# Optimization experiments

Hardware: AMD Instinct MI355X
Metric: run time of the kernel (lower is better)

Reference implementation:

```python
import jax, jax.numpy as jnp
import numpy as np

N = 100_000      # nodes
E = 800_000      # edges
NF = 32          # node_feature_size
EF = 32          # edge_feature_size
L = 64           # layer_size
ENTRY = NF + EF          # 64, input width of node_mlp_1
SECOND = NF + L          # 96, input width of node_mlp_2
SLOPE = 0.1              # leakiness
EPS = 1e-5               # BatchNorm1d eps


def _bn(h, g, b):
    # BatchNorm1d in training mode: batch mean, biased variance
    m = h.mean(0)
    v = ((h - m) ** 2).mean(0)
    return (h - m) * jax.lax.rsqrt(v + EPS) * g + b


def _lrelu(h):
    return jnp.where(h > 0, h, SLOPE * h)


def setup_inputs() -> dict:
    key = jax.random.key(0)
    ks = jax.random.split(key, 16)

    def w(k, i, o):
        return (jax.random.normal(k, (i, o), jnp.float32) / np.float32(np.sqrt(i)))

    def bvec(k, o):
        return jax.random.normal(k, (o,), jnp.float32) * 0.01

    inp = {
        "x": jax.random.normal(ks[0], (N, NF), jnp.float32),
        "edge_index": jax.random.randint(ks[1], (2, E), 0, N),
        "edge_attr": jax.random.normal(ks[2], (E, EF), jnp.float32),
        "u": jax.random.normal(ks[3], (1, 4), jnp.float32),
        "batch": jnp.zeros((N,), jnp.int32),
        # node_mlp_1 params
        "m1_g1": jnp.ones((ENTRY,), jnp.float32), "m1_b1": jnp.zeros((ENTRY,), jnp.float32),
        "m1_w1": w(ks[4], ENTRY, L), "m1_c1": bvec(ks[5], L),
        "m1_g2": jnp.ones((L,), jnp.float32), "m1_b2": jnp.zeros((L,), jnp.float32),
        "m1_w2": w(ks[6], L, L), "m1_c2": bvec(ks[7], L),
        "m1_g3": jnp.ones((L,), jnp.float32), "m1_b3": jnp.zeros((L,), jnp.float32),
        "m1_w3": w(ks[8], L, L), "m1_c3": bvec(ks[9], L),
        # node_mlp_2 params
        "m2_g1": jnp.ones((SECOND,), jnp.float32), "m2_b1": jnp.zeros((SECOND,), jnp.float32),
        "m2_w1": w(ks[10], SECOND, SECOND), "m2_c1": bvec(ks[11], SECOND),
        "m2_g2": jnp.ones((SECOND,), jnp.float32), "m2_b2": jnp.zeros((SECOND,), jnp.float32),
        "m2_w2": w(ks[12], SECOND, SECOND), "m2_c2": bvec(ks[13], SECOND),
        "m2_g3": jnp.ones((SECOND,), jnp.float32), "m2_b3": jnp.zeros((SECOND,), jnp.float32),
        "m2_w3": w(ks[14], SECOND, NF), "m2_c3": bvec(ks[15], NF),
    }
    return inp


def reference(x, edge_index, edge_attr, u, batch,
              m1_g1, m1_b1, m1_w1, m1_c1,
              m1_g2, m1_b2, m1_w2, m1_c2,
              m1_g3, m1_b3, m1_w3, m1_c3,
              m2_g1, m2_b1, m2_w1, m2_c1,
              m2_g2, m2_b2, m2_w2, m2_c2,
              m2_g3, m2_b3, m2_w3, m2_c3):
    row, col = edge_index[0], edge_index[1]
    # gather source node features, concat with edge features  [E, ENTRY]
    h = jnp.concatenate([x[row], edge_attr], axis=1)
    # node_mlp_1: BN -> Linear -> LReLU -> BN -> Linear -> LReLU -> BN -> Linear
    h = _lrelu(_bn(h, m1_g1, m1_b1) @ m1_w1 + m1_c1)
    h = _lrelu(_bn(h, m1_g2, m1_b2) @ m1_w2 + m1_c2)
    h = _bn(h, m1_g3, m1_b3) @ m1_w3 + m1_c3
    # scatter-sum back to destination nodes  [N, L]
    agg = jax.ops.segment_sum(h, col, num_segments=x.shape[0])
    # node_mlp_2 on [x, agg]  [N, SECOND]
    h2 = jnp.concatenate([x, agg], axis=1)
    h2 = _lrelu(_bn(h2, m2_g1, m2_b1) @ m2_w1 + m2_c1)
    h2 = _lrelu(_bn(h2, m2_g2, m2_b2) @ m2_w2 + m2_c2)
    out = _bn(h2, m2_g3, m2_b3) @ m2_w3 + m2_c3  # [N, NF]
    return out
```

## Files before the change

### kernel.cpp

```cpp
#include <hip/hip_runtime.h>


typedef unsigned short u16;
typedef __bf16  bf16x8  __attribute__((ext_vector_type(8)));
typedef float   floatx4 __attribute__((ext_vector_type(4)));

#define NBIN 8

__device__ __forceinline__ float bf2f(u16 u) {
  union { float f; unsigned int i; } v; v.i = ((unsigned int)u) << 16; return v.f;
}
__device__ __forceinline__ u16 f2bf(float f) {
  union { float f; unsigned int i; } v; v.f = f;
  unsigned int x = v.i;
  return (u16)((x + 0x7fffu + ((x >> 16) & 1u)) >> 16);
}
__device__ __forceinline__ bf16x8 ldb8(const u16* p) {
  return *reinterpret_cast<const bf16x8*>(p);
}
__device__ __forceinline__ floatx4 mfma16(bf16x8 a, bf16x8 b, floatx4 c) {
  return __builtin_amdgcn_mfma_f32_16x16x32_bf16(a, b, c, 0, 0, 0);
}
__device__ __forceinline__ float loadf(const void* p, long idx, int mode) {
  return mode ? bf2f(((const u16*)p)[idx]) : ((const float*)p)[idx];
}
__device__ __forceinline__ bf16x8 load8(const void* p, long idx, int mode) {
  if (mode) return ldb8((const u16*)p + idx);
  const float* f = (const float*)p + idx;
  bf16x8 r;
#pragma unroll
  for (int j = 0; j < 8; j++) r[j] = (__bf16)f[j];
  return r;
}

__global__ void detect_kernel(const u16* __restrict__ x, int* __restrict__ modep) {
  __shared__ int cnt;
  if (threadIdx.x == 0) cnt = 0;
  __syncthreads();
  int weird = 0;
  for (int i = threadIdx.x; i < 1024; i += blockDim.x) {
    unsigned e = (x[i] >> 7) & 0xFFu;
    if (e == 0xFFu || e >= 0x90u || (e != 0u && e < 0x60u)) weird++;
  }
  atomicAdd(&cnt, weird);
  __syncthreads();
  if (threadIdx.x == 0) *modep = (cnt > 128) ? 0 : 1;
}
// ... 17 lines not shown
  __syncthreads();
  int src = 0;
  for (int off = 1; off < 1024; off <<= 1) {
    int t = tmp[src][tid];
    if (tid >= off) t += tmp[src][tid - off];
    tmp[1 - src][tid] = t;
    src = 1 - src;
    __syncthreads();
  }
  if (i < n) excl[i] = tmp[src][tid] - v;
  if (tid == 1023) bsum[blockIdx.x] = tmp[src][1023];
}

__global__ void scan2_kernel(int* __restrict__ bsum, int nb,
                             int* __restrict__ offsets, int N, int E) {
  if (threadIdx.x == 0) {
    int run = 0;
    for (int i = 0; i < nb; i++) { int v = bsum[i]; bsum[i] = run; run += v; }
    offsets[N] = E;
  }
}

__global__ void scan3_kernel(int* __restrict__ offsets, const int* __restrict__ bsum,
                             int n, int* __restrict__ cursor) {
  int i = blockIdx.x * 1024 + threadIdx.x;
  if (i < n) {
    int v = offsets[i] + bsum[blockIdx.x];
    offsets[i] = v;
    cursor[i] = v;
  }
}

__global__ void scatter_kernel(const int* __restrict__ col, int E,
                               int* __restrict__ cursor, int* __restrict__ ipos,
                               int* __restrict__ nodeof) {
  for (int e = blockIdx.x * blockDim.x + threadIdx.x; e < E;
       e += gridDim.x * blockDim.x) {
    int d = col[e];
    int pos = atomicAdd(&cursor[d], 1);
    ipos[e] = pos;
    nodeof[pos] = d;
  }
}

__global__ void statsXW_kernel(const void* __restrict__ x, const int* __restrict__ odeg,
                               int N, float* __restrict__ stats0,
                               float* __restrict__ statsB0,
                               const int* __restrict__ modep) {
  const int mode = *modep;
  const int c = threadIdx.x & 31, rs = threadIdx.x >> 5;
  float s = 0.f, q = 0.f, ws = 0.f, wq = 0.f;
  for (long r = (long)blockIdx.x * 8 + rs; r < N; r += (long)gridDim.x * 8) {
    float v = loadf(x, r * 32 + c, mode);
    float w = (float)odeg[r];
    s += v; q += v * v;
    ws += w * v; wq += w * v * v;
  }
  __shared__ float sm[4][256];
  sm[0][threadIdx.x] = s; sm[1][threadIdx.x] = q;
  sm[2][threadIdx.x] = ws; sm[3][threadIdx.x] = wq;
  __syncthreads();
  if (threadIdx.x < 32) {
    for (int i = 1; i < 8; i++) {
      s  += sm[0][i * 32 + c]; q  += sm[1][i * 32 + c];
      ws += sm[2][i * 32 + c]; wq += sm[3][i * 32 + c];
    }
    const int bin = blockIdx.x & (NBIN - 1);
    atomicAdd(statsB0 + bin * 192 + c, s);
    atomicAdd(statsB0 + bin * 192 + 96 + c, q);
    atomicAdd(stats0 + bin * 128 + c, ws);
    atomicAdd(stats0 + bin * 128 + 64 + c, wq);
  }
}

__global__ void statsEA_kernel(const void* __restrict__ ea, int E,
                               float* __restrict__ stats,
                               const int* __restrict__ modep) {
  const int mode = *modep;
  const int cg = threadIdx.x & 3;
  const int rsub = threadIdx.x >> 2;
  float s[8], q[8];
#pragma unroll
  for (int j = 0; j < 8; j++) { s[j] = 0.f; q[j] = 0.f; }
  for (long r = (long)blockIdx.x * 64 + rsub; r < E; r += (long)gridDim.x * 64) {
    if (mode) {
      bf16x8 v = ldb8((const u16*)ea + r * 32 + cg * 8);
#pragma unroll
      for (int j = 0; j < 8; j++) { float f = (float)v[j]; s[j] += f; q[j] += f * f; }
    } else {
      const float* p = (const float*)ea + r * 32 + cg * 8;
      float4 a = *(const float4*)p;
      float4 b = *(const float4*)(p + 4);
      float f0[8] = {a.x, a.y, a.z, a.w, b.x, b.y, b.z, b.w};
#pragma unroll
      for (int j = 0; j < 8; j++) { s[j] += f0[j]; q[j] += f0[j] * f0[j]; }
    }
  }
  const int lane = threadIdx.x & 63;
#pragma unroll
  for (int st = 4; st < 64; st <<= 1) {
#pragma unroll
    for (int j = 0; j < 8; j++) {
      s[j] += __shfl_xor(s[j], st, 64);
      q[j] += __shfl_xor(q[j], st, 64);
    }
  }
  if (lane < 4) {
    float* o = stats + (blockIdx.x & (NBIN - 1)) * 128;
#pragma unroll
    for (int j = 0; j < 8; j++) {
      atomicAdd(o + 32 + lane * 8 + j, s[j]);
      atomicAdd(o + 96 + lane * 8 + j, q[j]);
    }
  }
}

__global__ void fold_kernel(const float* __restrict__ stats, float inv_rows,
                            const void* __restrict__ g, const void* __restrict__ b,
                            const void* __restrict__ W, const void* __restrict__ c,
                            int K, int OUT,
                            u16* __restrict__ Wpack, float* __restrict__ biasOut,
                            const int* __restrict__ modep) {
  const int mode = *modep;
  __shared__ float s_s[96], s_off[96];
  __shared__ float wlds[9216];
  const int tid = threadIdx.x;
  const int tot = K * OUT;
  for (int i = tid; i < tot; i += blockDim.x) wlds[i] = loadf(W, i, mode);
  if (tid < K) {
    float sum = 0.f, sq = 0.f;
    for (int p = 0; p < NBIN; p++) {
      sum += stats[p * 2 * K + tid];
      sq  += stats[p * 2 * K + K + tid];
    }
    float m   = sum * inv_rows;
    float var = sq * inv_rows - m * m;
    float s   = loadf(g, tid, mode) * rsqrtf(var + 1e-5f);
    s_s[tid]  = s;
    s_off[tid] = loadf(b, tid, mode) - m * s;
  }
  __syncthreads();
  for (int n = tid; n < OUT; n += blockDim.x) {
    float acc = loadf(c, n, mode);
    for (int k = 0; k < K; k++) acc += s_off[k] * wlds[k * OUT + n];
    biasOut[n] = acc;
  }
  const int H = K / 32, T = OUT / 16;
  const int total = T * H * 64 * 8;
  for (int i = tid; i < total; i += blockDim.x) {
    int j = i & 7, lane = (i >> 3) & 63, th = i >> 9;
    int h = th % H, t = th / H;
    int k = h * 32 + (lane >> 4) * 8 + j;
    int n = t * 16 + (lane & 15);
    Wpack[i] = f2bf(s_s[k] * wlds[k * OUT + n]);
  }
}


__global__ __launch_bounds__(256) void gemm1_kernel(
    const void* __restrict__ x, const void* __restrict__ ea,
    const int* __restrict__ erow, const int* __restrict__ ipos,
    const u16* __restrict__ Wp, const float* __restrict__ bias,
    u16* __restrict__ hout, int E,
    float* __restrict__ statsOut, const int* __restrict__ modep) {
  const int mode = *modep;
  const int lane = threadIdx.x & 63, wave = threadIdx.x >> 6;
  const int q = lane >> 4, r = lane & 15;
  const long wbase = (long)blockIdx.x * 256 + wave * 64;
  bf16x8 bfr[4][2];
#pragma unroll
  for (int t = 0; t < 4; t++)
#pragma unroll
    for (int h = 0; h < 2; h++)
      bfr[t][h] = ldb8(Wp + ((t * 2 + h) * 64 + lane) * 8);
  float bv[4];
#pragma unroll
  for (int t = 0; t < 4; t++) bv[t] = bias[t * 16 + r];
  float s_[4] = {0, 0, 0, 0}, q_[4] = {0, 0, 0, 0};
#pragma unroll
  for (int r4 = 0; r4 < 4; r4++) {
    const long row0 = wbase + r4 * 16;
    long e = row0 + r; if (e > E - 1) e = E - 1;
    int src = erow[e];
    bf16x8 a0 = load8(x, (long)src * 32 + q * 8, mode);
    bf16x8 a1 = load8(ea, e * 32 + q * 8, mode);
    floatx4 acc[4];
#pragma unroll
    for (int t = 0; t < 4; t++) {
      acc[t] = (floatx4){bv[t], bv[t], bv[t], bv[t]};
      acc[t] = mfma16(a0, bfr[t][0], acc[t]);
      acc[t] = mfma16(a1, bfr[t][1], acc[t]);
    }
#pragma unroll
    for (int gi = 0; gi < 4; gi++) {
      long row = row0 + q * 4 + gi;
      if (row < E) {
        long p = ipos[row];
#pragma unroll
        for (int t = 0; t < 4; t++) {
          float v = acc[t][gi];
          v = v > 0.f ? v : 0.1f * v;
          u16 st = f2bf(v);
          hout[p * 64 + t * 16 + r] = st;
          float vv = bf2f(st);
          s_[t] += vv; q_[t] += vv * vv;
        }
      }
    }
  }
  __shared__ float sm[512];
#pragma unroll
  for (int t = 0; t < 4; t++) {
    float s = s_[t], qq = q_[t];
    s  += __shfl_xor(s, 16, 64);  s  += __shfl_xor(s, 32, 64);
    qq += __shfl_xor(qq, 16, 64); qq += __shfl_xor(qq, 32, 64);
    if (lane < 16) { sm[wave * 128 + t * 16 + lane] = s; sm[wave * 128 + 64 + t * 16 + lane] = qq; }
  }
  __syncthreads();
  if (threadIdx.x < 128) {
    int which = threadIdx.x >> 6, c = threadIdx.x & 63;
    float v = 0.f;
    for (int w = 0; w < 4; w++) v += sm[w * 128 + which * 64 + c];
    atomicAdd(statsOut + (blockIdx.x & (NBIN - 1)) * 128 + which * 64 + c, v);
  }
}

__global__ __launch_bounds__(256) void gemm2_kernel(
    const u16* __restrict__ hin, const u16* __restrict__ Wp,
    const float* __restrict__ bias, int E,
    float* __restrict__ statsOut,
    const int* __restrict__ offs, const int* __restrict__ nodeof,
    float* __restrict__ s_e) {
  const int lane = threadIdx.x & 63, wave = threadIdx.x >> 6;
  const int q = lane >> 4, r = lane & 15;
  const long bbase = (long)blockIdx.x * 256;
  const long wbase = bbase + wave * 64;
  __shared__ u16 hs[256 * 64];
  __shared__ float sm[512];
  bf16x8 bfr[4][2];
#pragma unroll
  for (int t = 0; t < 4; t++)
#pragma unroll
    for (int h = 0; h < 2; h++)
      bfr[t][h] = ldb8(Wp + ((t * 2 + h) * 64 + lane) * 8);
  float bv[4];
#pragma unroll
  for (int t = 0; t < 4; t++) bv[t] = bias[t * 16 + r];
  float s_[4] = {0, 0, 0, 0}, q_[4] = {0, 0, 0, 0};
#pragma unroll
  for (int r4 = 0; r4 < 4; r4++) {
    const long row0 = wbase + r4 * 16;
    long e = row0 + r; if (e > E - 1) e = E - 1;
    bf16x8 a0 = ldb8(hin + e * 64 + q * 8);
    bf16x8 a1 = ldb8(hin + e * 64 + 32 + q * 8);
    floatx4 acc[4];
#pragma unroll
    for (int t = 0; t < 4; t++) {
      acc[t] = (floatx4){bv[t], bv[t], bv[t], bv[t]};
      acc[t] = mfma16(a0, bfr[t][0], acc[t]);
      acc[t] = mfma16(a1, bfr[t][1], acc[t]);
    }
    const int lbase = wave * 64 + r4 * 16;
// ... 11 lines not shown
          float vv = bf2f(st);
          s_[t] += vv; q_[t] += vv * vv;
        }
      }
    }
  }
#pragma unroll
  for (int t = 0; t < 4; t++) {
    float s = s_[t], qq = q_[t];
    s  += __shfl_xor(s, 16, 64);  s  += __shfl_xor(s, 32, 64);
    qq += __shfl_xor(qq, 16, 64); qq += __shfl_xor(qq, 32, 64);
    if (lane < 16) { sm[wave * 128 + t * 16 + lane] = s; sm[wave * 128 + 64 + t * 16 + lane] = qq; }
  }
  __syncthreads();
  if (threadIdx.x < 128) {
    int which = threadIdx.x >> 6, c = threadIdx.x & 63;
    float v = 0.f;
    for (int w = 0; w < 4; w++) v += sm[w * 128 + which * 64 + c];
    atomicAdd(statsOut + (blockIdx.x & (NBIN - 1)) * 128 + which * 64 + c, v);
  }
  const long blockEnd = (bbase + 256 < (long)E) ? bbase + 256 : (long)E;
  const int first = nodeof[bbase];
  const int last  = nodeof[blockEnd - 1];
  for (int idx = first + wave; idx <= last; idx += 4) {
    int st = offs[idx], en = offs[idx + 1];
    long cs = st < bbase ? bbase : (long)st;
    long ce = (long)en > blockEnd ? blockEnd : (long)en;
    if (cs >= ce) continue;
    float acc = 0.f;
    for (long i = cs - bbase; i < ce - bbase; i++)
      acc += bf2f(hs[i * 64 + (lane ^ (int)(((i >> 2) & 3) << 4))]);
    if ((long)st >= bbase && (long)en <= blockEnd)
      s_e[(long)idx * 64 + lane] = acc;
    else
      atomicAdd(s_e + (long)idx * 64 + lane, acc);
  }
}

__global__ __launch_bounds__(256) void gemmAgg_kernel(
    const float* __restrict__ s_e, const int* __restrict__ deg,
    const u16* __restrict__ Wp, const float* __restrict__ bias,
    float* __restrict__ agg, int N, float* __restrict__ statsOut) {
  const int lane = threadIdx.x & 63, wave = threadIdx.x >> 6;
  const int q = lane >> 4, r = lane & 15;
  const long wbase = (long)blockIdx.x * 256 + wave * 64;
  bf16x8 bfr[4][2];
#pragma unroll
  for (int t = 0; t < 4; t++)
#pragma unroll
    for (int h = 0; h < 2; h++)
      bfr[t][h] = ldb8(Wp + ((t * 2 + h) * 64 + lane) * 8);
  float bv[4];
#pragma unroll
  for (int t = 0; t < 4; t++) bv[t] = bias[t * 16 + r];
  float s_[4] = {0, 0, 0, 0}, q_[4] = {0, 0, 0, 0};
#pragma unroll
  for (int r4 = 0; r4 < 4; r4++) {
    const long row0 = wbase + r4 * 16;
    long m = row0 + r;
    long mm = m < N ? m : (long)N - 1;
    bf16x8 a0, a1;
    {
      const float* ap = s_e + mm * 64 + q * 8;
#pragma unroll
      for (int j = 0; j < 8; j++) a0[j] = (__bf16)ap[j];
#pragma unroll
      for (int j = 0; j < 8; j++) a1[j] = (__bf16)ap[32 + j];
    }
    floatx4 acc[4];
#pragma unroll
    for (int t = 0; t < 4; t++) {
      acc[t] = (floatx4){0.f, 0.f, 0.f, 0.f};
      acc[t] = mfma16(a0, bfr[t][0], acc[t]);
      acc[t] = mfma16(a1, bfr[t][1], acc[t]);
    }
#pragma unroll
    for (int gi = 0; gi < 4; gi++) {
      long row = row0 + q * 4 + gi;
      if (row < N) {
        float d = (float)deg[row];
#pragma unroll
        for (int t = 0; t < 4; t++) {
          float v = acc[t][gi] + d * bv[t];
          agg[row * 64 + t * 16 + r] = v;
          s_[t] += v; q_[t] += v * v;
        }
      }
    }
  }
  __shared__ float sm[512];
#pragma unroll
  for (int t = 0; t < 4; t++) {
    float s = s_[t], qq = q_[t];
    s  += __shfl_xor(s, 16, 64);  s  += __shfl_xor(s, 32, 64);
    qq += __shfl_xor(qq, 16, 64); qq += __shfl_xor(qq, 32, 64);
    if (lane < 16) { sm[wave * 128 + t * 16 + lane] = s; sm[wave * 128 + 64 + t * 16 + lane] = qq; }
  }
  __syncthreads();
  if (threadIdx.x < 128) {
    int which = threadIdx.x >> 6, c = threadIdx.x & 63;
    float v = 0.f;
    for (int w = 0; w < 4; w++) v += sm[w * 128 + which * 64 + c];
    atomicAdd(statsOut + (blockIdx.x & (NBIN - 1)) * 192 + which * 96 + 32 + c, v);
  }
}


__global__ __launch_bounds__(256) void gemmB1_kernel(
    const void* __restrict__ x, const float* __restrict__ agg,
    const u16* __restrict__ Wp, const float* __restrict__ bias,
    u16* __restrict__ hout, int N, float* __restrict__ statsOut,
    const int* __restrict__ modep) {
  const int mode = *modep;
  const int lane = threadIdx.x & 63, wave = threadIdx.x >> 6;
  const int q = lane >> 4, r = lane & 15;
  const long wbase = (long)blockIdx.x * 256 + wave * 64;
  bf16x8 bfr[6][3];
#pragma unroll
  for (int t = 0; t < 6; t++)
#pragma unroll
    for (int h = 0; h < 3; h++)
      bfr[t][h] = ldb8(Wp + ((t * 3 + h) * 64 + lane) * 8);
  float bv[6];
#pragma unroll
  for (int t = 0; t < 6; t++) bv[t] = bias[t * 16 + r];
  float s_[6] = {0, 0, 0, 0, 0, 0}, q_[6] = {0, 0, 0, 0, 0, 0};
#pragma unroll
  for (int r4 = 0; r4 < 4; r4++) {
    const long row0 = wbase + r4 * 16;
    long m = row0 + r;
    long mm = m < N ? m : (long)N - 1;
    bf16x8 a0 = load8(x, mm * 32 + q * 8, mode);
    bf16x8 a1, a2;
    {
      const float* ap = agg + mm * 64 + q * 8;
#pragma unroll
      for (int j = 0; j < 8; j++) a1[j] = (__bf16)ap[j];
#pragma unroll
      for (int j = 0; j < 8; j++) a2[j] = (__bf16)ap[32 + j];
    }
    floatx4 acc[6];
#pragma unroll
    for (int t = 0; t < 6; t++) {
      acc[t] = (floatx4){bv[t], bv[t], bv[t], bv[t]};
      acc[t] = mfma16(a0, bfr[t][0], acc[t]);
      acc[t] = mfma16(a1, bfr[t][1], acc[t]);
      acc[t] = mfma16(a2, bfr[t][2], acc[t]);
    }
#pragma unroll
    for (int t = 0; t < 6; t++)
#pragma unroll
      for (int gi = 0; gi < 4; gi++) {
        long row = row0 + q * 4 + gi;
        if (row < N) {
          float v = acc[t][gi];
          v = v > 0.f ? v : 0.1f * v;
          u16 st = f2bf(v);
          hout[row * 96 + t * 16 + r] = st;
          float vv = bf2f(st);
          s_[t] += vv; q_[t] += vv * vv;
        }
      }
  }
  __shared__ float sm[768];
#pragma unroll
  for (int t = 0; t < 6; t++) {
    float s = s_[t], qq = q_[t];
    s  += __shfl_xor(s, 16, 64);  s  += __shfl_xor(s, 32, 64);
    qq += __shfl_xor(qq, 16, 64); qq += __shfl_xor(qq, 32, 64);
    if (lane < 16) { sm[wave * 192 + t * 16 + lane] = s; sm[wave * 192 + 96 + t * 16 + lane] = qq; }
  }
  __syncthreads();
  if (threadIdx.x < 192) {
    int which = threadIdx.x / 96, c = threadIdx.x % 96;
    float v = 0.f;
    for (int w = 0; w < 4; w++) v += sm[w * 192 + which * 96 + c];
    atomicAdd(statsOut + (blockIdx.x & (NBIN - 1)) * 192 + which * 96 + c, v);
  }
}

__global__ __launch_bounds__(256) void gemmB2_kernel(
    const u16* __restrict__ hin, const u16* __restrict__ Wp,
    const float* __restrict__ bias, u16* __restrict__ hout, int N,
    float* __restrict__ statsOut) {
  const int lane = threadIdx.x & 63, wave = threadIdx.x >> 6;
  const int q = lane >> 4, r = lane & 15;
  const long wbase = (long)blockIdx.x * 256 + wave * 64;
  bf16x8 bfr[6][3];
#pragma unroll
  for (int t = 0; t < 6; t++)
#pragma unroll
    for (int h = 0; h < 3; h++)
      bfr[t][h] = ldb8(Wp + ((t * 3 + h) * 64 + lane) * 8);
  float bv[6];
#pragma unroll
  for (int t = 0; t < 6; t++) bv[t] = bias[t * 16 + r];
  float s_[6] = {0, 0, 0, 0, 0, 0}, q_[6] = {0, 0, 0, 0, 0, 0};
#pragma unroll
  for (int r4 = 0; r4 < 4; r4++) {
    const long row0 = wbase + r4 * 16;
    long m = row0 + r;
    long mm = m < N ? m : (long)N - 1;
    bf16x8 a0 = ldb8(hin + mm * 96 + q * 8);
    bf16x8 a1 = ldb8(hin + mm * 96 + 32 + q * 8);
    bf16x8 a2 = ldb8(hin + mm * 96 + 64 + q * 8);
    floatx4 acc[6];
#pragma unroll
    for (int t = 0; t < 6; t++) {
      acc[t] = (floatx4){bv[t], bv[t], bv[t], bv[t]};
      acc[t] = mfma16(a0, bfr[t][0], acc[t]);
      acc[t] = mfma16(a1, bfr[t][1], acc[t]);
// ... 2 lines not shown
#pragma unroll
    for (int t = 0; t < 6; t++)
#pragma unroll
      for (int gi = 0; gi < 4; gi++) {
        long row = row0 + q * 4 + gi;
        if (row < N) {
          float v = acc[t][gi];
          v = v > 0.f ? v : 0.1f * v;
          u16 st = f2bf(v);
          hout[row * 96 + t * 16 + r] = st;
          float vv = bf2f(st);
          s_[t] += vv; q_[t] += vv * vv;
        }
      }
  }
  __shared__ float sm[768];
#pragma unroll
  for (int t = 0; t < 6; t++) {
    float s = s_[t], qq = q_[t];
    s  += __shfl_xor(s, 16, 64);  s  += __shfl_xor(s, 32, 64);
    qq += __shfl_xor(qq, 16, 64); qq += __shfl_xor(qq, 32, 64);
    if (lane < 16) { sm[wave * 192 + t * 16 + lane] = s; sm[wave * 192 + 96 + t * 16 + lane] = qq; }
  }
  __syncthreads();
  if (threadIdx.x < 192) {
    int which = threadIdx.x / 96, c = threadIdx.x % 96;
    float v = 0.f;
    for (int w = 0; w < 4; w++) v += sm[w * 192 + which * 96 + c];
    atomicAdd(statsOut + (blockIdx.x & (NBIN - 1)) * 192 + which * 96 + c, v);
  }
}

__global__ __launch_bounds__(256) void gemmB3_kernel(
    const u16* __restrict__ hin, const u16* __restrict__ Wp,
    const float* __restrict__ bias, void* __restrict__ outv, int N,
    const int* __restrict__ modep) {
  const int mode = *modep;
  const int lane = threadIdx.x & 63, wave = threadIdx.x >> 6;
  const int q = lane >> 4, r = lane & 15;
  const long wbase = (long)blockIdx.x * 256 + wave * 64;
  bf16x8 bfr[2][3];
#pragma unroll
  for (int t = 0; t < 2; t++)
#pragma unroll
    for (int h = 0; h < 3; h++)
      bfr[t][h] = ldb8(Wp + ((t * 3 + h) * 64 + lane) * 8);
  float bv[2];
#pragma unroll
  for (int t = 0; t < 2; t++) bv[t] = bias[t * 16 + r];
#pragma unroll
  for (int r4 = 0; r4 < 4; r4++) {
    const long row0 = wbase + r4 * 16;
    long m = row0 + r;
    long mm = m < N ? m : (long)N - 1;
    bf16x8 a0 = ldb8(hin + mm * 96 + q * 8);
    bf16x8 a1 = ldb8(hin + mm * 96 + 32 + q * 8);
    bf16x8 a2 = ldb8(hin + mm * 96 + 64 + q * 8);
    floatx4 acc[2];
#pragma unroll
    for (int t = 0; t < 2; t++) {
      acc[t] = (floatx4){bv[t], bv[t], bv[t], bv[t]};
      acc[t] = mfma16(a0, bfr[t][0], acc[t]);
      acc[t] = mfma16(a1, bfr[t][1], acc[t]);
      acc[t] = mfma16(a2, bfr[t][2], acc[t]);
// ... 26 lines not shown
  const void *m1_g2 = d_in[9],  *m1_b2 = d_in[10];
  const void *m1_w2 = d_in[11], *m1_c2 = d_in[12];
  const void *m1_g3 = d_in[13], *m1_b3 = d_in[14];
  const void *m1_w3 = d_in[15], *m1_c3 = d_in[16];
  const void *m2_g1 = d_in[17], *m2_b1 = d_in[18];
  const void *m2_w1 = d_in[19], *m2_c1 = d_in[20];
  const void *m2_g2 = d_in[21], *m2_b2 = d_in[22];
  const void *m2_w2 = d_in[23], *m2_c2 = d_in[24];
  const void *m2_g3 = d_in[25], *m2_b3 = d_in[26];
  const void *m2_w3 = d_in[27], *m2_c3 = d_in[28];

  char* w = (char*)d_ws;
  int*   modep  = (int*)w;   w += 16;
  u16*   h_s    = (u16*)w;   w += (size_t)E * 64 * 2;
  u16*   h2b    = (u16*)w;   w += (size_t)N * 96 * 2;
  float* agg    = (float*)w; w += (size_t)N * 64 * 4;
  int*   offs   = (int*)w;   w += ((size_t)N + 4) * 4;
  int*   cursor = (int*)w;   w += ((size_t)N + 4) * 4;
  int*   ipos   = (int*)w;   w += (size_t)E * 4;
  int*   nodeof = (int*)w;   w += (size_t)E * 4;
  int*   bsum   = (int*)w;   w += 1024 * 4;
  float* s_e    = (float*)w; w += (size_t)N * 64 * 4;
  int*   deg    = (int*)w;   w += (size_t)N * 4;
  int*   odeg   = (int*)w;   w += (size_t)N * 4;
  float* stats0 = (float*)w; w += NBIN * 128 * 4;
  float* stats1 = (float*)w; w += NBIN * 128 * 4;
  float* stats2 = (float*)w; w += NBIN * 128 * 4;
  float* statsB0= (float*)w; w += NBIN * 192 * 4;
  float* statsB1= (float*)w; w += NBIN * 192 * 4;
  float* statsB2= (float*)w; w += NBIN * 192 * 4;
  const size_t zero_bytes = (size_t)N * 64 * 4 + (size_t)N * 8 +
                            NBIN * (128 * 3 + 192 * 3) * 4;
  u16*   Wp1    = (u16*)w;   w += 4096 * 2;
  float* bias1  = (float*)w; w += 64 * 4;
  u16*   Wp2    = (u16*)w;   w += 4096 * 2;
  float* bias2  = (float*)w; w += 64 * 4;
  u16*   Wp3    = (u16*)w;   w += 4096 * 2;
  float* bias3  = (float*)w; w += 64 * 4;
  u16*   WpB1   = (u16*)w;   w += 9216 * 2;
  float* biasB1 = (float*)w; w += 96 * 4;
  u16*   WpB2   = (u16*)w;   w += 9216 * 2;
  float* biasB2 = (float*)w; w += 96 * 4;
  u16*   WpB3   = (u16*)w;   w += 3072 * 2;
  float* biasB3 = (float*)w; w += 32 * 4;

  const int* erow = eidx;
  const int* ecol = eidx + E;
  const float invE = 1.0f / (float)E, invN = 1.0f / (float)N;
  const int gA = (E + 255) / 256, gB = (N + 255) / 256;
  const int nb = (N + 1023) / 1024;

  detect_kernel<<<1, 256, 0, stream>>>((const u16*)x, modep);
  hipMemsetAsync(s_e, 0, zero_bytes, stream);

  count2_kernel<<<1024, 256, 0, stream>>>(erow, ecol, E, odeg, deg);
  scan1_kernel<<<nb, 1024, 0, stream>>>(deg, N, offs, bsum);
  scan2_kernel<<<1, 64, 0, stream>>>(bsum, nb, offs, N, E);
  scan3_kernel<<<nb, 1024, 0, stream>>>(offs, bsum, N, cursor);
  scatter_kernel<<<1024, 256, 0, stream>>>(ecol, E, cursor, ipos, nodeof);

  statsXW_kernel<<<512, 256, 0, stream>>>(x, odeg, N, stats0, statsB0, modep);
  statsEA_kernel<<<512, 256, 0, stream>>>(ea, E, stats0, modep);

  fold_kernel<<<1, 256, 0, stream>>>(stats0, invE, m1_g1, m1_b1, m1_w1, m1_c1,
                                     64, 64, Wp1, bias1, modep);
  gemm1_kernel<<<gA, 256, 0, stream>>>(x, ea, erow, ipos, Wp1, bias1, h_s, E,
                                       stats1, modep);
  fold_kernel<<<1, 256, 0, stream>>>(stats1, invE, m1_g2, m1_b2, m1_w2, m1_c2,
                                     64, 64, Wp2, bias2, modep);
  gemm2_kernel<<<gA, 256, 0, stream>>>(h_s, Wp2, bias2, E, stats2,
                                       offs, nodeof, s_e);

  fold_kernel<<<1, 256, 0, stream>>>(stats2, invE, m1_g3, m1_b3, m1_w3, m1_c3,
                                     64, 64, Wp3, bias3, modep);
  gemmAgg_kernel<<<gB, 256, 0, stream>>>(s_e, deg, Wp3, bias3, agg, N, statsB0);

  fold_kernel<<<1, 256, 0, stream>>>(statsB0, invN, m2_g1, m2_b1, m2_w1, m2_c1,
                                     96, 96, WpB1, biasB1, modep);
  gemmB1_kernel<<<gB, 256, 0, stream>>>(x, agg, WpB1, biasB1, h2b, N,
                                        statsB1, modep);
  fold_kernel<<<1, 256, 0, stream>>>(statsB1, invN, m2_g2, m2_b2, m2_w2, m2_c2,
                                     96, 96, WpB2, biasB2, modep);
  gemmB2_kernel<<<gB, 256, 0, stream>>>(h2b, WpB2, biasB2, h2b, N, statsB2);
  fold_kernel<<<1, 256, 0, stream>>>(statsB2, invN, m2_g3, m2_b3, m2_w3, m2_c3,
                                     96, 32, WpB3, biasB3, modep);
  gemmB3_kernel<<<gB, 256, 0, stream>>>(h2b, WpB3, biasB3, d_out, N, modep);
}
```

Before: 698.0 us.

## Fold BN into each GEMM block, merge stats kernels, pre-convert inputs to bf16

Removes the six single-block fold kernels: every GEMM block now recomputes the BN-folded, packed weights and bias in shared memory from the batch statistics. The two input-statistics kernels are merged into one launch that also writes bf16 copies of x and edge_attr, so the gather GEMM reads narrower data. Other changes are a parallel scan2, prefetching gather indices in gemm1, and storing agg as bf16. This cuts launch count and serial single-block stalls, but each block repeats the weight-folding work and the bf16 agg may lose precision.

```diff
diff --git a/kernel.cpp b/kernel.cpp
--- a/kernel.cpp
+++ b/kernel.cpp
@@ -31,6 +31,45 @@
 #pragma unroll
   for (int j = 0; j < 8; j++) r[j] = (__bf16)f[j];
   return r;
+}
+
+__device__ __forceinline__ void fold_block(
+    const float* __restrict__ stats, float inv_rows,
+    const void* __restrict__ g, const void* __restrict__ b,
+    const void* __restrict__ W, const void* __restrict__ c,
+    int K, int OUT, int mode,
+    u16* wlds, u16* wpack, float* s_s, float* s_off, float* sbias) {
+  const int tid = threadIdx.x;
+  const int tot = K * OUT;
+  for (int i = tid; i < tot; i += 256)
+    wlds[i] = mode ? ((const u16*)W)[i] : f2bf(((const float*)W)[i]);
+  if (tid < K) {
+    float sum = 0.f, sq = 0.f;
+    for (int p = 0; p < NBIN; p++) {
+      sum += stats[p * 2 * K + tid];
+      sq  += stats[p * 2 * K + K + tid];
+    }
+    float m = sum * inv_rows, var = sq * inv_rows - m * m;
+    float s = loadf(g, tid, mode) * rsqrtf(var + 1e-5f);
+    s_s[tid] = s;
+    s_off[tid] = loadf(b, tid, mode) - m * s;
+  }
+  __syncthreads();
+  if (tid < OUT) {
+    float acc = loadf(c, tid, mode);
+    for (int k = 0; k < K; k++) acc += s_off[k] * bf2f(wlds[k * OUT + tid]);
+    sbias[tid] = acc;
+  }
+  const int H = K >> 5, T = OUT >> 4;
+  const int total = T * H * 512;
+  for (int i = tid; i < total; i += 256) {
+    int j = i & 7, lane = (i >> 3) & 63, th = i >> 9;
+    int h = th % H, t = th / H;
+    int k = h * 32 + ((lane >> 4) << 3) + j;
+    int n = (t << 4) + (lane & 15);
+    wpack[i] = f2bf(s_s[k] * bf2f(wlds[k * OUT + n]));
+  }
+  __syncthreads();
 }
 
 __global__ void detect_kernel(const u16* __restrict__ x, int* __restrict__ modep) {
@@ -78,11 +117,21 @@
 
 __global__ void scan2_kernel(int* __restrict__ bsum, int nb,
                              int* __restrict__ offsets, int N, int E) {
-  if (threadIdx.x == 0) {
-    int run = 0;
-    for (int i = 0; i < nb; i++) { int v = bsum[i]; bsum[i] = run; run += v; }
-    offsets[N] = E;
-  }
+  __shared__ int tmp[2][1024];
+  const int tid = threadIdx.x;
+  int v = (tid < nb) ? bsum[tid] : 0;
+  tmp[0][tid] = v;
+  __syncthreads();
+  int src = 0;
+  for (int off = 1; off < 1024; off <<= 1) {
+    int t = tmp[src][tid];
+    if (tid >= off) t += tmp[src][tid - off];
+    tmp[1 - src][tid] = t;
+    src = 1 - src;
+    __syncthreads();
+  }
+  if (tid < nb) bsum[tid] = tmp[src][tid] - v;
+  if (tid == 0) offsets[N] = E;
 }
 
 __global__ void scan3_kernel(int* __restrict__ offsets, const int* __restrict__ bsum,
@@ -107,127 +156,100 @@
   }
 }
 
-__global__ void statsXW_kernel(const void* __restrict__ x, const int* __restrict__ odeg,
-                               int N, float* __restrict__ stats0,
-                               float* __restrict__ statsB0,
-                               const int* __restrict__ modep) {
+__global__ void stats_in_kernel(const void* __restrict__ x,
+                                const int* __restrict__ odeg, int N,
+                                const void* __restrict__ ea, int E,
+                                float* __restrict__ stats0,
+                                float* __restrict__ statsB0,
+                                u16* __restrict__ xb, u16* __restrict__ eab,
+                                const int* __restrict__ modep) {
   const int mode = *modep;
-  const int c = threadIdx.x & 31, rs = threadIdx.x >> 5;
-  float s = 0.f, q = 0.f, ws = 0.f, wq = 0.f;
-  for (long r = (long)blockIdx.x * 8 + rs; r < N; r += (long)gridDim.x * 8) {
-    float v = loadf(x, r * 32 + c, mode);
-    float w = (float)odeg[r];
-    s += v; q += v * v;
-    ws += w * v; wq += w * v * v;
-  }
-  __shared__ float sm[4][256];
-  sm[0][threadIdx.x] = s; sm[1][threadIdx.x] = q;
-  sm[2][threadIdx.x] = ws; sm[3][threadIdx.x] = wq;
-  __syncthreads();
-  if (threadIdx.x < 32) {
-    for (int i = 1; i < 8; i++) {
-      s  += sm[0][i * 32 + c]; q  += sm[1][i * 32 + c];
-      ws += sm[2][i * 32 + c]; wq += sm[3][i * 32 + c];
-    }
-    const int bin = blockIdx.x & (NBIN - 1);
-    atomicAdd(statsB0 + bin * 192 + c, s);
-    atomicAdd(statsB0 + bin * 192 + 96 + c, q);
-    atomicAdd(stats0 + bin * 128 + c, ws);
-    atomicAdd(stats0 + bin * 128 + 64 + c, wq);
-  }
-}
-
-__global__ void statsEA_kernel(const void* __restrict__ ea, int E,
-                               float* __restrict__ stats,
-                               const int* __restrict__ modep) {
-  const int mode = *modep;
-  const int cg = threadIdx.x & 3;
-  const int rsub = threadIdx.x >> 2;
-  float s[8], q[8];
-#pragma unroll
-  for (int j = 0; j < 8; j++) { s[j] = 0.f; q[j] = 0.f; }
-  for (long r = (long)blockIdx.x * 64 + rsub; r < E; r += (long)gridDim.x * 64) {
-    if (mode) {
-      bf16x8 v = ldb8((const u16*)ea + r * 32 + cg * 8);
-#pragma unroll
-      for (int j = 0; j < 8; j++) { float f = (float)v[j]; s[j] += f; q[j] += f * f; }
-    } else {
-      const float* p = (const float*)ea + r * 32 + cg * 8;
-      float4 a = *(const float4*)p;
-      float4 b = *(const float4*)(p + 4);
-      float f0[8] = {a.x, a.y, a.z, a.w, b.x, b.y, b.z, b.w};
+  if (blockIdx.x < 512) {
+    const int c = threadIdx.x & 31, rs = threadIdx.x >> 5;
+    float s = 0.f, q = 0.f, ws = 0.f, wq = 0.f;
+    for (long rr = (long)blockIdx.x * 8 + rs; rr < N; rr += 512 * 8) {
+      float v = loadf(x, rr * 32 + c, mode);
+      float w = (float)odeg[rr];
+      xb[rr * 32 + c] = f2bf(v);
+      s += v; q += v * v; ws += w * v; wq += w * v * v;
+    }
+    __shared__ float sm[4][256];
+    sm[0][threadIdx.x] = s;  sm[1][threadIdx.x] = q;
+    sm[2][threadIdx.x] = ws; sm[3][threadIdx.x] = wq;
+    __syncthreads();
+    if (threadIdx.x < 32) {
+      for (int i = 1; i < 8; i++) {
+        s  += sm[0][i * 32 + c]; q  += sm[1][i * 32 + c];
+        ws += sm[2][i * 32 + c]; wq += sm[3][i * 32 + c];
+      }
+      const int bin = blockIdx.x & (NBIN - 1);
+      atomicAdd(statsB0 + bin * 192 + c, s);
+      atomicAdd(statsB0 + bin * 192 + 96 + c, q);
+      atomicAdd(stats0 + bin * 128 + c, ws);
+      atomicAdd(stats0 + bin * 128 + 64 + c, wq);
+    }
+  } else {
+    const int bid = blockIdx.x - 512;
+    const int cg = threadIdx.x & 3, rsub = threadIdx.x >> 2;
+    float s[8], q[8];
+#pragma unroll
+    for (int j = 0; j < 8; j++) { s[j] = 0.f; q[j] = 0.f; }
+    for (long rr = (long)bid * 64 + rsub; rr < E; rr += 512 * 64) {
+      float f0[8];
+      if (mode) {
+        bf16x8 v = ldb8((const u16*)ea + rr * 32 + cg * 8);
+#pragma unroll
+        for (int j = 0; j < 8; j++) f0[j] = (float)v[j];
+      } else {
+        const float* p = (const float*)ea + rr * 32 + cg * 8;
+        float4 a = *(const float4*)p;
+        float4 b = *(const float4*)(p + 4);
+        f0[0]=a.x; f0[1]=a.y; f0[2]=a.z; f0[3]=a.w;
+        f0[4]=b.x; f0[5]=b.y; f0[6]=b.z; f0[7]=b.w;
+      }
+      if (eab) {
+        bf16x8 o;
+#pragma unroll
+        for (int j = 0; j < 8; j++) o[j] = (__bf16)f0[j];
+        *reinterpret_cast<bf16x8*>(eab + rr * 32 + cg * 8) = o;
+      }
 #pragma unroll
       for (int j = 0; j < 8; j++) { s[j] += f0[j]; q[j] += f0[j] * f0[j]; }
     }
-  }
-  const int lane = threadIdx.x & 63;
-#pragma unroll
-  for (int st = 4; st < 64; st <<= 1) {
-#pragma unroll
-    for (int j = 0; j < 8; j++) {
-      s[j] += __shfl_xor(s[j], st, 64);
-      q[j] += __shfl_xor(q[j], st, 64);
-    }
-  }
-  if (lane < 4) {
-    float* o = stats + (blockIdx.x & (NBIN - 1)) * 128;
-#pragma unroll
-    for (int j = 0; j < 8; j++) {
-      atomicAdd(o + 32 + lane * 8 + j, s[j]);
-      atomicAdd(o + 96 + lane * 8 + j, q[j]);
-    }
-  }
-}
-
-__global__ void fold_kernel(const float* __restrict__ stats, float inv_rows,
-                            const void* __restrict__ g, const void* __restrict__ b,
-                            const void* __restrict__ W, const void* __restrict__ c,
-                            int K, int OUT,
-                            u16* __restrict__ Wpack, float* __restrict__ biasOut,
-                            const int* __restrict__ modep) {
-  const int mode = *modep;
-  __shared__ float s_s[96], s_off[96];
-  __shared__ float wlds[9216];
-  const int tid = threadIdx.x;
-  const int tot = K * OUT;
-  for (int i = tid; i < tot; i += blockDim.x) wlds[i] = loadf(W, i, mode);
-  if (tid < K) {
-    float sum = 0.f, sq = 0.f;
-    for (int p = 0; p < NBIN; p++) {
-      sum += stats[p * 2 * K + tid];
-      sq  += stats[p * 2 * K + K + tid];
-    }
-    float m   = sum * inv_rows;
-    float var = sq * inv_rows - m * m;
-    float s   = loadf(g, tid, mode) * rsqrtf(var + 1e-5f);
-    s_s[tid]  = s;
-    s_off[tid] = loadf(b, tid, mode) - m * s;
-  }
-  __syncthreads();
-  for (int n = tid; n < OUT; n += blockDim.x) {
-    float acc = loadf(c, n, mode);
-    for (int k = 0; k < K; k++) acc += s_off[k] * wlds[k * OUT + n];
-    biasOut[n] = acc;
-  }
-  const int H = K / 32, T = OUT / 16;
-  const int total = T * H * 64 * 8;
-  for (int i = tid; i < total; i += blockDim.x) {
-    int j = i & 7, lane = (i >> 3) & 63, th = i >> 9;
-    int h = th % H, t = th / H;
-    int k = h * 32 + (lane >> 4) * 8 + j;
-    int n = t * 16 + (lane & 15);
-    Wpack[i] = f2bf(s_s[k] * wlds[k * OUT + n]);
-  }
-}
-
+    const int lane = threadIdx.x & 63;
+#pragma unroll
+    for (int st = 4; st < 64; st <<= 1) {
+#pragma unroll
+      for (int j = 0; j < 8; j++) {
+        s[j] += __shfl_xor(s[j], st, 64);
+        q[j] += __shfl_xor(q[j], st, 64);
+      }
+    }
+    if (lane < 4) {
+      float* o = stats0 + (blockIdx.x & (NBIN - 1)) * 128;
+#pragma unroll
+      for (int j = 0; j < 8; j++) {
+        atomicAdd(o + 32 + lane * 8 + j, s[j]);
+        atomicAdd(o + 96 + lane * 8 + j, q[j]);
+      }
+    }
+  }
+}
 
 __global__ __launch_bounds__(256) void gemm1_kernel(
-    const void* __restrict__ x, const void* __restrict__ ea,
+    const u16* __restrict__ xb, const void* __restrict__ ea, int eamode,
     const int* __restrict__ erow, const int* __restrict__ ipos,
-    const u16* __restrict__ Wp, const float* __restrict__ bias,
+    const float* __restrict__ stats0, float invE,
+    const void* __restrict__ g, const void* __restrict__ b,
+    const void* __restrict__ W, const void* __restrict__ c,
     u16* __restrict__ hout, int E,
     float* __restrict__ statsOut, const int* __restrict__ modep) {
+  __shared__ u16 wlds[4096], wpack[4096];
+  __shared__ float s_s[64], s_off[64], sbias[64];
+  __shared__ float sm[512];
   const int mode = *modep;
+  const int em = eamode >= 0 ? eamode : mode;
+  fold_block(stats0, invE, g, b, W, c, 64, 64, mode, wlds, wpack, s_s, s_off, sbias);
   const int lane = threadIdx.x & 63, wave = threadIdx.x >> 6;
   const int q = lane >> 4, r = lane & 15;
   const long wbase = (long)blockIdx.x * 256 + wave * 64;
@@ -236,30 +258,38 @@
   for (int t = 0; t < 4; t++)
 #pragma unroll
     for (int h = 0; h < 2; h++)
-      bfr[t][h] = ldb8(Wp + ((t * 2 + h) * 64 + lane) * 8);
+      bfr[t][h] = *reinterpret_cast<const bf16x8*>(wpack + ((t * 2 + h) * 64 + lane) * 8);
   float bv[4];
 #pragma unroll
-  for (int t = 0; t < 4; t++) bv[t] = bias[t * 16 + r];
+  for (int t = 0; t < 4; t++) bv[t] = sbias[t * 16 + r];
+  bf16x8 a0v[4], a1v[4];
+  int pv[4][4];
+#pragma unroll
+  for (int r4 = 0; r4 < 4; r4++) {
+    long e = wbase + r4 * 16 + r; if (e > E - 1) e = E - 1;
+    int src = erow[e];
+    a0v[r4] = ldb8(xb + (long)src * 32 + q * 8);
+    a1v[r4] = load8(ea, e * 32 + q * 8, em);
+#pragma unroll
+    for (int gi = 0; gi < 4; gi++) {
+      long row = wbase + r4 * 16 + q * 4 + gi;
+      pv[r4][gi] = (row < E) ? ipos[row] : -1;
+    }
+  }
   float s_[4] = {0, 0, 0, 0}, q_[4] = {0, 0, 0, 0};
 #pragma unroll
   for (int r4 = 0; r4 < 4; r4++) {
-    const long row0 = wbase + r4 * 16;
-    long e = row0 + r; if (e > E - 1) e = E - 1;
-    int src = erow[e];
-    bf16x8 a0 = load8(x, (long)src * 32 + q * 8, mode);
-    bf16x8 a1 = load8(ea, e * 32 + q * 8, mode);
     floatx4 acc[4];
 #pragma unroll
     for (int t = 0; t < 4; t++) {
       acc[t] = (floatx4){bv[t], bv[t], bv[t], bv[t]};
-      acc[t] = mfma16(a0, bfr[t][0], acc[t]);
-      acc[t] = mfma16(a1, bfr[t][1], acc[t]);
+      acc[t] = mfma16(a0v[r4], bfr[t][0], acc[t]);
+      acc[t] = mfma16(a1v[r4], bfr[t][1], acc[t]);
     }
 #pragma unroll
     for (int gi = 0; gi < 4; gi++) {
-      long row = row0 + q * 4 + gi;
-      if (row < E) {
-        long p = ipos[row];
+      long p = pv[r4][gi];
+      if (p >= 0) {
 #pragma unroll
         for (int t = 0; t < 4; t++) {
           float v = acc[t][gi];
@@ -272,7 +302,6 @@
       }
     }
   }
-  __shared__ float sm[512];
 #pragma unroll
   for (int t = 0; t < 4; t++) {
     float s = s_[t], qq = q_[t];
@@ -282,34 +311,40 @@
   }
   __syncthreads();
   if (threadIdx.x < 128) {
-    int which = threadIdx.x >> 6, c = threadIdx.x & 63;
+    int which = threadIdx.x >> 6, cc = threadIdx.x & 63;
     float v = 0.f;
-    for (int w = 0; w < 4; w++) v += sm[w * 128 + which * 64 + c];
-    atomicAdd(statsOut + (blockIdx.x & (NBIN - 1)) * 128 + which * 64 + c, v);
+    for (int w = 0; w < 4; w++) v += sm[w * 128 + which * 64 + cc];
+    atomicAdd(statsOut + (blockIdx.x & (NBIN - 1)) * 128 + which * 64 + cc, v);
   }
 }
 
 __global__ __launch_bounds__(256) void gemm2_kernel(
-    const u16* __restrict__ hin, const u16* __restrict__ Wp,
-    const float* __restrict__ bias, int E,
-    float* __restrict__ statsOut,
+    const u16* __restrict__ hin,
+    const float* __restrict__ stats1, float invE,
+    const void* __restrict__ g, const void* __restrict__ b,
+    const void* __restrict__ W, const void* __restrict__ c,
+    int E, float* __restrict__ statsOut,
     const int* __restrict__ offs, const int* __restrict__ nodeof,
-    float* __restrict__ s_e) {
+    float* __restrict__ s_e, const int* __restrict__ modep) {
+  __shared__ u16 wlds[4096], wpack[4096];
+  __shared__ float s_s[64], s_off[64], sbias[64];
+  __shared__ u16 hs[256 * 64];
+  __shared__ float sm[512];
+  const int mode = *modep;
+  fold_block(stats1, invE, g, b, W, c, 64, 64, mode, wlds, wpack, s_s, s_off, sbias);
   const int lane = threadIdx.x & 63, wave = threadIdx.x >> 6;
   const int q = lane >> 4, r = lane & 15;
   const long bbase = (long)blockIdx.x * 256;
   const long wbase = bbase + wave * 64;
-  __shared__ u16 hs[256 * 64];
-  __shared__ float sm[512];
   bf16x8 bfr[4][2];
 #pragma unroll
   for (int t = 0; t < 4; t++)
 #pragma unroll
     for (int h = 0; h < 2; h++)
-      bfr[t][h] = ldb8(Wp + ((t * 2 + h) * 64 + lane) * 8);
+      bfr[t][h] = *reinterpret_cast<const bf16x8*>(wpack + ((t * 2 + h) * 64 + lane) * 8);
   float bv[4];
 #pragma unroll
-  for (int t = 0; t < 4; t++) bv[t] = bias[t * 16 + r];
+  for (int t = 0; t < 4; t++) bv[t] = sbias[t * 16 + r];
   float s_[4] = {0, 0, 0, 0}, q_[4] = {0, 0, 0, 0};
 #pragma unroll
   for (int r4 = 0; r4 < 4; r4++) {
@@ -351,10 +386,10 @@
   }
   __syncthreads();
   if (threadIdx.x < 128) {
-    int which = threadIdx.x >> 6, c = threadIdx.x & 63;
+    int which = threadIdx.x >> 6, cc = threadIdx.x & 63;
     float v = 0.f;
-    for (int w = 0; w < 4; w++) v += sm[w * 128 + which * 64 + c];
-    atomicAdd(statsOut + (blockIdx.x & (NBIN - 1)) * 128 + which * 64 + c, v);
+    for (int w = 0; w < 4; w++) v += sm[w * 128 + which * 64 + cc];
+    atomicAdd(statsOut + (blockIdx.x & (NBIN - 1)) * 128 + which * 64 + cc, v);
   }
   const long blockEnd = (bbase + 256 < (long)E) ? bbase + 256 : (long)E;
   const int first = nodeof[bbase];
@@ -376,8 +411,16 @@
 
 __global__ __launch_bounds__(256) void gemmAgg_kernel(
     const float* __restrict__ s_e, const int* __restrict__ deg,
-    const u16* __restrict__ Wp, const float* __restrict__ bias,
-    float* __restrict__ agg, int N, float* __restrict__ statsOut) {
+    const float* __restrict__ stats2, float invE,
+    const void* __restrict__ g, const void* __restrict__ b,
+    const void* __restrict__ W, const void* __restrict__ c,
+    u16* __restrict__ agg_b, int N, float* __restrict__ statsOut,
+    const int* __restrict__ modep) {
+  __shared__ u16 wlds[4096], wpack[4096];
+  __shared__ float s_s[64], s_off[64], sbias[64];
+  __shared__ float sm[512];
+  const int mode = *modep;
+  fold_block(stats2, invE, g, b, W, c, 64, 64, mode, wlds, wpack, s_s, s_off, sbias);
   const int lane = threadIdx.x & 63, wave = threadIdx.x >> 6;
   const int q = lane >> 4, r = lane & 15;
   const long wbase = (long)blockIdx.x * 256 + wave * 64;
@@ -386,10 +429,10 @@
   for (int t = 0; t < 4; t++)
 #pragma unroll
     for (int h = 0; h < 2; h++)
-      bfr[t][h] = ldb8(Wp + ((t * 2 + h) * 64 + lane) * 8);
+      bfr[t][h] = *reinterpret_cast<const bf16x8*>(wpack + ((t * 2 + h) * 64 + lane) * 8);
   float bv[4];
 #pragma unroll
-  for (int t = 0; t < 4; t++) bv[t] = bias[t * 16 + r];
+  for (int t = 0; t < 4; t++) bv[t] = sbias[t * 16 + r];
   float s_[4] = {0, 0, 0, 0}, q_[4] = {0, 0, 0, 0};
 #pragma unroll
   for (int r4 = 0; r4 < 4; r4++) {
@@ -419,13 +462,12 @@
 #pragma unroll
         for (int t = 0; t < 4; t++) {
           float v = acc[t][gi] + d * bv[t];
-          agg[row * 64 + t * 16 + r] = v;
+          agg_b[row * 64 + t * 16 + r] = f2bf(v);
           s_[t] += v; q_[t] += v * v;
         }
       }
     }
   }
-  __shared__ float sm[512];
 #pragma unroll
   for (int t = 0; t < 4; t++) {
     float s = s_[t], qq = q_[t];
@@ -435,20 +477,25 @@
   }
   __syncthreads();
   if (threadIdx.x < 128) {
-    int which = threadIdx.x >> 6, c = threadIdx.x & 63;
+    int which = threadIdx.x >> 6, cc = threadIdx.x & 63;
     float v = 0.f;
-    for (int w = 0; w < 4; w++) v += sm[w * 128 + which * 64 + c];
-    atomicAdd(statsOut + (blockIdx.x & (NBIN - 1)) * 192 + which * 96 + 32 + c, v);
-  }
-}
-
+    for (int w = 0; w < 4; w++) v += sm[w * 128 + which * 64 + cc];
+    atomicAdd(statsOut + (blockIdx.x & (NBIN - 1)) * 192 + which * 96 + 32 + cc, v);
+  }
+}
 
 __global__ __launch_bounds__(256) void gemmB1_kernel(
-    const void* __restrict__ x, const float* __restrict__ agg,
-    const u16* __restrict__ Wp, const float* __restrict__ bias,
+    const u16* __restrict__ xb, const u16* __restrict__ agg_b,
+    const float* __restrict__ statsB0, float invN,
+    const void* __restrict__ g, const void* __restrict__ b,
+    const void* __restrict__ W, const void* __restrict__ c,
     u16* __restrict__ hout, int N, float* __restrict__ statsOut,
     const int* __restrict__ modep) {
+  __shared__ u16 wlds[9216], wpack[9216];
+  __shared__ float s_s[96], s_off[96], sbias[96];
+  __shared__ float sm[768];
   const int mode = *modep;
+  fold_block(statsB0, invN, g, b, W, c, 96, 96, mode, wlds, wpack, s_s, s_off, sbias);
   const int lane = threadIdx.x & 63, wave = threadIdx.x >> 6;
   const int q = lane >> 4, r = lane & 15;
   const long wbase = (long)blockIdx.x * 256 + wave * 64;
@@ -457,25 +504,19 @@
   for (int t = 0; t < 6; t++)
 #pragma unroll
     for (int h = 0; h < 3; h++)
-      bfr[t][h] = ldb8(Wp + ((t * 3 + h) * 64 + lane) * 8);
+      bfr[t][h] = *reinterpret_cast<const bf16x8*>(wpack + ((t * 3 + h) * 64 + lane) * 8);
   float bv[6];
 #pragma unroll
-  for (int t = 0; t < 6; t++) bv[t] = bias[t * 16 + r];
+  for (int t = 0; t < 6; t++) bv[t] = sbias[t * 16 + r];
   float s_[6] = {0, 0, 0, 0, 0, 0}, q_[6] = {0, 0, 0, 0, 0, 0};
 #pragma unroll
   for (int r4 = 0; r4 < 4; r4++) {
     const long row0 = wbase + r4 * 16;
     long m = row0 + r;
     long mm = m < N ? m : (long)N - 1;
-    bf16x8 a0 = load8(x, mm * 32 + q * 8, mode);
-    bf16x8 a1, a2;
-    {
-      const float* ap = agg + mm * 64 + q * 8;
-#pragma unroll
-      for (int j = 0; j < 8; j++) a1[j] = (__bf16)ap[j];
-#pragma unroll
-      for (int j = 0; j < 8; j++) a2[j] = (__bf16)ap[32 + j];
-    }
+    bf16x8 a0 = ldb8(xb + mm * 32 + q * 8);
+    bf16x8 a1 = ldb8(agg_b + mm * 64 + q * 8);
+    bf16x8 a2 = ldb8(agg_b + mm * 64 + 32 + q * 8);
     floatx4 acc[6];
 #pragma unroll
     for (int t = 0; t < 6; t++) {
@@ -499,7 +540,6 @@
         }
       }
   }
-  __shared__ float sm[768];
 #pragma unroll
   for (int t = 0; t < 6; t++) {
     float s = s_[t], qq = q_[t];
@@ -509,17 +549,25 @@
   }
   __syncthreads();
   if (threadIdx.x < 192) {
-    int which = threadIdx.x / 96, c = threadIdx.x % 96;
+    int which = threadIdx.x / 96, cc = threadIdx.x % 96;
     float v = 0.f;
-    for (int w = 0; w < 4; w++) v += sm[w * 192 + which * 96 + c];
-    atomicAdd(statsOut + (blockIdx.x & (NBIN - 1)) * 192 + which * 96 + c, v);
+    for (int w = 0; w < 4; w++) v += sm[w * 192 + which * 96 + cc];
+    atomicAdd(statsOut + (blockIdx.x & (NBIN - 1)) * 192 + which * 96 + cc, v);
   }
 }
 
 __global__ __launch_bounds__(256) void gemmB2_kernel(
-    const u16* __restrict__ hin, const u16* __restrict__ Wp,
-    const float* __restrict__ bias, u16* __restrict__ hout, int N,
-    float* __restrict__ statsOut) {
+    const u16* __restrict__ hin,
+    const float* __restrict__ statsB1, float invN,
+    const void* __restrict__ g, const void* __restrict__ b,
+    const void* __restrict__ W, const void* __restrict__ c,
+    u16* __restrict__ hout, int N, float* __restrict__ statsOut,
+    const int* __restrict__ modep) {
+  __shared__ u16 wlds[9216], wpack[9216];
+  __shared__ float s_s[96], s_off[96], sbias[96];
+  __shared__ float sm[768];
+  const int mode = *modep;
+  fold_block(statsB1, invN, g, b, W, c, 96, 96, mode, wlds, wpack, s_s, s_off, sbias);
   const int lane = threadIdx.x & 63, wave = threadIdx.x >> 6;
   const int q = lane >> 4, r = lane & 15;
   const long wbase = (long)blockIdx.x * 256 + wave * 64;
@@ -528,10 +576,10 @@
   for (int t = 0; t < 6; t++)
 #pragma unroll
     for (int h = 0; h < 3; h++)
-      bfr[t][h] = ldb8(Wp + ((t * 3 + h) * 64 + lane) * 8);
+      bfr[t][h] = *reinterpret_cast<const bf16x8*>(wpack + ((t * 3 + h) * 64 + lane) * 8);
   float bv[6];
 #pragma unroll
-  for (int t = 0; t < 6; t++) bv[t] = bias[t * 16 + r];
+  for (int t = 0; t < 6; t++) bv[t] = sbias[t * 16 + r];
   float s_[6] = {0, 0, 0, 0, 0, 0}, q_[6] = {0, 0, 0, 0, 0, 0};
 #pragma unroll
   for (int r4 = 0; r4 < 4; r4++) {
@@ -564,7 +612,6 @@
         }
       }
   }
-  __shared__ float sm[768];
 #pragma unroll
   for (int t = 0; t < 6; t++) {
     float s = s_[t], qq = q_[t];
@@ -574,18 +621,23 @@
   }
   __syncthreads();
   if (threadIdx.x < 192) {
-    int which = threadIdx.x / 96, c = threadIdx.x % 96;
+    int which = threadIdx.x / 96, cc = threadIdx.x % 96;
     float v = 0.f;
-    for (int w = 0; w < 4; w++) v += sm[w * 192 + which * 96 + c];
-    atomicAdd(statsOut + (blockIdx.x & (NBIN - 1)) * 192 + which * 96 + c, v);
+    for (int w = 0; w < 4; w++) v += sm[w * 192 + which * 96 + cc];
+    atomicAdd(statsOut + (blockIdx.x & (NBIN - 1)) * 192 + which * 96 + cc, v);
   }
 }
 
 __global__ __launch_bounds__(256) void gemmB3_kernel(
-    const u16* __restrict__ hin, const u16* __restrict__ Wp,
-    const float* __restrict__ bias, void* __restrict__ outv, int N,
-    const int* __restrict__ modep) {
+    const u16* __restrict__ hin,
+    const float* __restrict__ statsB2, float invN,
+    const void* __restrict__ g, const void* __restrict__ b,
+    const void* __restrict__ W, const void* __restrict__ c,
+    void* __restrict__ outv, int N, const int* __restrict__ modep) {
+  __shared__ u16 wlds[3072], wpack[3072];
+  __shared__ float s_s[96], s_off[96], sbias[32];
   const int mode = *modep;
+  fold_block(statsB2, invN, g, b, W, c, 96, 32, mode, wlds, wpack, s_s, s_off, sbias);
   const int lane = threadIdx.x & 63, wave = threadIdx.x >> 6;
   const int q = lane >> 4, r = lane & 15;
   const long wbase = (long)blockIdx.x * 256 + wave * 64;
@@ -594,10 +646,10 @@
   for (int t = 0; t < 2; t++)
 #pragma unroll
     for (int h = 0; h < 3; h++)
-      bfr[t][h] = ldb8(Wp + ((t * 3 + h) * 64 + lane) * 8);
+      bfr[t][h] = *reinterpret_cast<const bf16x8*>(wpack + ((t * 3 + h) * 64 + lane) * 8);
   float bv[2];
 #pragma unroll
-  for (int t = 0; t < 2; t++) bv[t] = bias[t * 16 + r];
+  for (int t = 0; t < 2; t++) bv[t] = sbias[t * 16 + r];
 #pragma unroll
   for (int r4 = 0; r4 < 4; r4++) {
     const long row0 = wbase + r4 * 16;
@@ -654,7 +706,8 @@
   int*   modep  = (int*)w;   w += 16;
   u16*   h_s    = (u16*)w;   w += (size_t)E * 64 * 2;
   u16*   h2b    = (u16*)w;   w += (size_t)N * 96 * 2;
-  float* agg    = (float*)w; w += (size_t)N * 64 * 4;
+  u16*   agg_b  = (u16*)w;   w += (size_t)N * 64 * 2;
+  u16*   xb     = (u16*)w;   w += (size_t)N * 32 * 2;
   int*   offs   = (int*)w;   w += ((size_t)N + 4) * 4;
   int*   cursor = (int*)w;   w += ((size_t)N + 4) * 4;
   int*   ipos   = (int*)w;   w += (size_t)E * 4;
@@ -671,18 +724,10 @@
   float* statsB2= (float*)w; w += NBIN * 192 * 4;
   const size_t zero_bytes = (size_t)N * 64 * 4 + (size_t)N * 8 +
                             NBIN * (128 * 3 + 192 * 3) * 4;
-  u16*   Wp1    = (u16*)w;   w += 4096 * 2;
-  float* bias1  = (float*)w; w += 64 * 4;
-  u16*   Wp2    = (u16*)w;   w += 4096 * 2;
-  float* bias2  = (float*)w; w += 64 * 4;
-  u16*   Wp3    = (u16*)w;   w += 4096 * 2;
-  float* bias3  = (float*)w; w += 64 * 4;
-  u16*   WpB1   = (u16*)w;   w += 9216 * 2;
-  float* biasB1 = (float*)w; w += 96 * 4;
-  u16*   WpB2   = (u16*)w;   w += 9216 * 2;
-  float* biasB2 = (float*)w; w += 96 * 4;
-  u16*   WpB3   = (u16*)w;   w += 3072 * 2;
-  float* biasB3 = (float*)w; w += 32 * 4;
+  const size_t eab_bytes = (size_t)E * 32 * 2;
+  const size_t used = (size_t)(w - (char*)d_ws);
+  const int use_eab = (ws_size >= used + eab_bytes) ? 1 : 0;
+  u16* eab = use_eab ? (u16*)w : nullptr;
 
   const int* erow = eidx;
   const int* ecol = eidx + E;
@@ -695,34 +740,32 @@
 
   count2_kernel<<<1024, 256, 0, stream>>>(erow, ecol, E, odeg, deg);
   scan1_kernel<<<nb, 1024, 0, stream>>>(deg, N, offs, bsum);
-  scan2_kernel<<<1, 64, 0, stream>>>(bsum, nb, offs, N, E);
+  scan2_kernel<<<1, 1024, 0, stream>>>(bsum, nb, offs, N, E);
   scan3_kernel<<<nb, 1024, 0, stream>>>(offs, bsum, N, cursor);
   scatter_kernel<<<1024, 256, 0, stream>>>(ecol, E, cursor, ipos, nodeof);
 
-  statsXW_kernel<<<512, 256, 0, stream>>>(x, odeg, N, stats0, statsB0, modep);
-  statsEA_kernel<<<512, 256, 0, stream>>>(ea, E, stats0, modep);
-
-  fold_kernel<<<1, 256, 0, stream>>>(stats0, invE, m1_g1, m1_b1, m1_w1, m1_c1,
-                                     64, 64, Wp1, bias1, modep);
-  gemm1_kernel<<<gA, 256, 0, stream>>>(x, ea, erow, ipos, Wp1, bias1, h_s, E,
-                                       stats1, modep);
-  fold_kernel<<<1, 256, 0, stream>>>(stats1, invE, m1_g2, m1_b2, m1_w2, m1_c2,
-                                     64, 64, Wp2, bias2, modep);
-  gemm2_kernel<<<gA, 256, 0, stream>>>(h_s, Wp2, bias2, E, stats2,
-                                       offs, nodeof, s_e);
-
-  fold_kernel<<<1, 256, 0, stream>>>(stats2, invE, m1_g3, m1_b3, m1_w3, m1_c3,
-                                     64, 64, Wp3, bias3, modep);
-  gemmAgg_kernel<<<gB, 256, 0, stream>>>(s_e, deg, Wp3, bias3, agg, N, statsB0);
-
-  fold_kernel<<<1, 256, 0, stream>>>(statsB0, invN, m2_g1, m2_b1, m2_w1, m2_c1,
-                                     96, 96, WpB1, biasB1, modep);
-  gemmB1_kernel<<<gB, 256, 0, stream>>>(x, agg, WpB1, biasB1, h2b, N,
-                                        statsB1, modep);
-  fold_kernel<<<1, 256, 0, stream>>>(statsB1, invN, m2_g2, m2_b2, m2_w2, m2_c2,
-                                     96, 96, WpB2, biasB2, modep);
-  gemmB2_kernel<<<gB, 256, 0, stream>>>(h2b, WpB2, biasB2, h2b, N, statsB2);
-  fold_kernel<<<1, 256, 0, stream>>>(statsB2, invN, m2_g3, m2_b3, m2_w3, m2_c3,
-                                     96, 32, WpB3, biasB3, modep);
-  gemmB3_kernel<<<gB, 256, 0, stream>>>(h2b, WpB3, biasB3, d_out, N, modep);
-}
+  stats_in_kernel<<<1024, 256, 0, stream>>>(x, odeg, N, ea, E,
+                                            stats0, statsB0, xb, eab, modep);
+
+  gemm1_kernel<<<gA, 256, 0, stream>>>(
+      xb, use_eab ? (const void*)eab : ea, use_eab ? 1 : -1,
+      erow, ipos, stats0, invE, m1_g1, m1_b1, m1_w1, m1_c1,
+      h_s, E, stats1, modep);
+  gemm2_kernel<<<gA, 256, 0, stream>>>(
+      h_s, stats1, invE, m1_g2, m1_b2, m1_w2, m1_c2,
+      E, stats2, offs, nodeof, s_e, modep);
+
+  gemmAgg_kernel<<<gB, 256, 0, stream>>>(
+      s_e, deg, stats2, invE, m1_g3, m1_b3, m1_w3, m1_c3,
+      agg_b, N, statsB0, modep);
+
+  gemmB1_kernel<<<gB, 256, 0, stream>>>(
+      xb, agg_b, statsB0, invN, m2_g1, m2_b1, m2_w1, m2_c1,
+      h2b, N, statsB1, modep);
+  gemmB2_kernel<<<gB, 256, 0, stream>>>(
+      h2b, statsB1, invN, m2_g2, m2_b2, m2_w2, m2_c2,
+      h2b, N, statsB2, modep);
+  gemmB3_kernel<<<gB, 256, 0, stream>>>(
+      h2b, statsB2, invN, m2_g3, m2_b3, m2_w3, m2_c3,
+      d_out, N, modep);
+}
```

Result: no change. 688.8 us (-1.3%).
